# Kernel tuning notes

Hardware: AMD Instinct MI355X
Metric: run time of the kernel (lower is better)

Reference implementation:

```python
import jax, jax.numpy as jnp
import numpy as np

NUM_SINK = 8   # cfg.SINKHORN_ITERS
MASS = 0.9     # marginal value used for a and b


def _graph_conv(x, W_enc, b_enc, W1, b1, W2, b2, k):
    # Node encoder
    h = jax.nn.relu(x @ W_enc + b_enc)                       # [G,M,D]
    # kNN in embedding space (per graph)
    sq = jnp.sum(h * h, axis=-1)                             # [G,M]
    d2 = sq[:, :, None] + sq[:, None, :] - 2.0 * jnp.einsum('gmd,gnd->gmn', h, h)
    d2 = d2 + jnp.eye(h.shape[1], dtype=h.dtype) * 1e9       # exclude self-loop
    _, idx = jax.lax.top_k(-d2, k)                           # [G,M,k]
    neigh = jax.vmap(lambda hg, ig: hg[ig])(h, idx)          # [G,M,k,D]
    hc = jnp.broadcast_to(h[:, :, None, :], neigh.shape)
    e = jnp.concatenate([hc, neigh - hc], axis=-1)           # [G,M,k,2D]
    e = jax.nn.relu(e @ W1 + b1)                             # edge embed
    e = e @ W2 + b2                                          # back to D
    return jnp.max(e, axis=2)                                # max-aggregate over neighbors


def _sinkhorn(cost, lam):
    # log-domain unrolled Sinkhorn, batched over graphs; a=b=0.9 marginals
    log_p = -cost / lam                                      # [G,M,N]
    log_m = jnp.log(jnp.asarray(MASS, cost.dtype))
    for _ in range(NUM_SINK - 1):
        log_p = log_p - (jax.nn.logsumexp(log_p, axis=2, keepdims=True) - log_m)
        log_p = log_p - (jax.nn.logsumexp(log_p, axis=1, keepdims=True) - log_m)
    log_p = log_p - (jax.nn.logsumexp(log_p, axis=2, keepdims=True) - log_m)
    return jnp.exp(log_p)


def setup_inputs() -> dict:
    key = jax.random.key(0)
    ks = jax.random.split(key, 6)
    G, M, D = 64, 256, 256
    E = 256  # edge embed size
    inp = {
        'tra_x': jax.random.normal(ks[0], (G, M, D), jnp.float32),
        'det_x': jax.random.normal(ks[1], (G, M, D), jnp.float32),
        'W_enc': jax.random.normal(ks[2], (D, D), jnp.float32) / np.sqrt(D),
        'b_enc': jnp.zeros((D,), jnp.float32),
        'W1': jax.random.normal(ks[3], (2 * D, E), jnp.float32) / np.sqrt(2 * D),
        'b1': jnp.zeros((E,), jnp.float32),
        'W2': jax.random.normal(ks[4], (E, D), jnp.float32) / np.sqrt(E),
        'b2': jnp.zeros((D,), jnp.float32),
        'eplison': jnp.zeros((1,), jnp.float32),
        'k': 16,
    }
    return inp


def reference(tra_x, det_x, W_enc, b_enc, W1, b1, W2, b2, eplison, k):
    tra = _graph_conv(tra_x, W_enc, b_enc, W1, b1, W2, b2, k)  # [G,M,D]
    det = _graph_conv(det_x, W_enc, b_enc, W1, b1, W2, b2, k)  # [G,N,D]
    corr = jnp.einsum('gmd,gnd->gmn', tra, det)
    n1 = jnp.linalg.norm(tra, axis=-1)                         # [G,M]
    n2 = jnp.linalg.norm(det, axis=-1)                         # [G,N]
    cost = -corr / (n1[:, :, None] * n2[:, None, :])
    lam = jnp.exp(eplison[0]) + 0.03
    return _sinkhorn(cost, lam)                                # [G,M,N]
```

## Files before the change

### kernel.cpp

```cpp
#include <hip/hip_runtime.h>
#include <math.h>

#define NG 64
#define NM 256
#define ND 256
#define NK 16
#define NR (NG * NM)
#define NB 32

#define MASSF 0.9f

typedef _Float16 f16;
typedef __attribute__((ext_vector_type(8))) _Float16 f16x8;
typedef __attribute__((ext_vector_type(4))) _Float16 f16x4;
typedef __attribute__((ext_vector_type(4))) float f32x4;
typedef __attribute__((ext_vector_type(4))) unsigned u32x4;

static __device__ __forceinline__ unsigned pkrelu(unsigned a, unsigned b) {
  unsigned r;
  asm("v_pk_add_f16 %0, %1, %2" : "=v"(r) : "v"(a), "v"(b));
  asm("v_pk_max_f16 %0, %1, %2" : "=v"(r) : "v"(r), "v"(0u));
  return r;
}

__global__ __launch_bounds__(256) void prep_k(const float* __restrict__ W1,
                                              const float* __restrict__ b1,
                                              const float* __restrict__ W2,
                                              f16* __restrict__ w2t, f16* __restrict__ w1cat,
                                              float* __restrict__ biascat) {
  const int b = blockIdx.x, k = threadIdx.x;
  if (b < 256) {
    w2t[b * 256 + k] = (f16)W2[(size_t)k * 256 + b];
  } else {
    const int n = b - 256;
    float v;
    if (n < 256)
      v = W1[(size_t)k * 256 + n] - W1[(size_t)(k + 256) * 256 + n];
    else
      v = W1[(size_t)(k + 256) * 256 + (n - 256)];
    w1cat[(size_t)n * 256 + k] = (f16)v;
    if (k == 0) biascat[n] = (n < 256) ? b1[n] : 0.f;
  }
}

__global__ __launch_bounds__(256) void gemm_nn2_k(const float* __restrict__ A,
                                                  const float* __restrict__ B,
                                                  const float* __restrict__ bias,
                                                  float* __restrict__ C,
                                                  f16* __restrict__ Cf) {
  __shared__ float As[2][16][68];
  __shared__ float Bs[2][16][128];
  const int tid = threadIdx.x;
  const int tx = tid & 15, ty = tid >> 4;
  const int m0 = blockIdx.y * 64, n0 = blockIdx.x * 128;
  const int arow = tid >> 2, akc = (tid & 3) * 4;
  const int bkr = tid >> 4, bcc = (tid & 15) * 4;
  float4 av, bv0, bv1;
  float acc[4][8] = {};
  auto gload = [&](int k0) {
    av = *(const float4*)&A[(size_t)(m0 + arow) * 256 + k0 + akc];
    bv0 = *(const float4*)&B[(size_t)(k0 + bkr) * 256 + n0 + bcc];
    bv1 = *(const float4*)&B[(size_t)(k0 + bkr) * 256 + n0 + 64 + bcc];
  };
  auto swrite = [&](int buf) {
    As[buf][akc + 0][arow] = av.x;
    As[buf][akc + 1][arow] = av.y;
    As[buf][akc + 2][arow] = av.z;
    As[buf][akc + 3][arow] = av.w;
    *(float4*)&Bs[buf][bkr][bcc] = bv0;
    *(float4*)&Bs[buf][bkr][64 + bcc] = bv1;
  };
  gload(0);
  swrite(0);
  __syncthreads();
  for (int s = 0; s < 16; ++s) {
    if (s < 15) gload((s + 1) * 16);
    const int buf = s & 1;
#pragma unroll
    for (int kk = 0; kk < 16; ++kk) {
      const float4 a0 = *(const float4*)&As[buf][kk][ty * 4];
      const float4 b0 = *(const float4*)&Bs[buf][kk][tx * 4];
      const float4 b1 = *(const float4*)&Bs[buf][kk][64 + tx * 4];
      const float aa[4] = {a0.x, a0.y, a0.z, a0.w};
      const float bb[8] = {b0.x, b0.y, b0.z, b0.w, b1.x, b1.y, b1.z, b1.w};
#pragma unroll
      for (int i = 0; i < 4; ++i)
#pragma unroll
        for (int j = 0; j < 8; ++j) acc[i][j] = fmaf(aa[i], bb[j], acc[i][j]);
    }
    if (s < 15) swrite((s + 1) & 1);
    __syncthreads();
  }
  const float4 bia0 = *(const float4*)&bias[n0 + tx * 4];
  const float4 bia1 = *(const float4*)&bias[n0 + 64 + tx * 4];
#pragma unroll
  for (int i = 0; i < 4; ++i) {
    const size_t row = (size_t)(m0 + ty * 4 + i);
    float4 o0 = {fmaxf(acc[i][0] + bia0.x, 0.f), fmaxf(acc[i][1] + bia0.y, 0.f),
                 fmaxf(acc[i][2] + bia0.z, 0.f), fmaxf(acc[i][3] + bia0.w, 0.f)};
    float4 o1 = {fmaxf(acc[i][4] + bia1.x, 0.f), fmaxf(acc[i][5] + bia1.y, 0.f),
                 fmaxf(acc[i][6] + bia1.z, 0.f), fmaxf(acc[i][7] + bia1.w, 0.f)};
    *(float4*)&C[row * 256 + n0 + tx * 4] = o0;
    *(float4*)&C[row * 256 + n0 + 64 + tx * 4] = o1;
    f16x4 h0 = {(f16)o0.x, (f16)o0.y, (f16)o0.z, (f16)o0.w};
    f16x4 h1 = {(f16)o1.x, (f16)o1.y, (f16)o1.z, (f16)o1.w};
    *(f16x4*)&Cf[row * 256 + n0 + tx * 4] = h0;
    *(f16x4*)&Cf[row * 256 + n0 + 64 + tx * 4] = h1;
  }
}

__global__ __launch_bounds__(256) void gemm_nt2_k(const float* __restrict__ h,
                                                  float* __restrict__ C,
                                                  float* __restrict__ sq) {
  const int flat0 = blockIdx.x + 2 * (blockIdx.y + 4 * blockIdx.z);
  const int flat = ((flat0 & 7) << 6) | (flat0 >> 3);
  const int bx = flat & 1, by = (flat >> 1) & 3, g = flat >> 3;
  if (bx == 0 && by >= 2) return;
  __shared__ float As[2][16][68];
  __shared__ float Bs[2][16][128];
  const float* Ag = h + (size_t)g * NM * ND;
  float* Cg = C + (size_t)g * NM * NM;
  const int tid = threadIdx.x;
  const int tx = tid & 15, ty = tid >> 4;
  const int m0 = by * 64, n0 = bx * 128;
  const int arow = tid >> 2, akc = (tid & 3) * 4;
  const int brow = tid >> 1, bkc = (tid & 1) * 8;
  float4 av, bva, bvb;
  float acc[4][8] = {};
  auto gload = [&](int k0) {
    av = *(const float4*)&Ag[(size_t)(m0 + arow) * 256 + k0 + akc];
    bva = *(const float4*)&Ag[(size_t)(n0 + brow) * 256 + k0 + bkc];
    bvb = *(const float4*)&Ag[(size_t)(n0 + brow) * 256 + k0 + bkc + 4];
  };
  auto swrite = [&](int buf) {
    As[buf][akc + 0][arow] = av.x;
    As[buf][akc + 1][arow] = av.y;
    As[buf][akc + 2][arow] = av.z;
    As[buf][akc + 3][arow] = av.w;
    Bs[buf][bkc + 0][brow] = bva.x;
    Bs[buf][bkc + 1][brow] = bva.y;
    Bs[buf][bkc + 2][brow] = bva.z;
    Bs[buf][bkc + 3][brow] = bva.w;
    Bs[buf][bkc + 4][brow] = bvb.x;
    Bs[buf][bkc + 5][brow] = bvb.y;
    Bs[buf][bkc + 6][brow] = bvb.z;
    Bs[buf][bkc + 7][brow] = bvb.w;
  };
  gload(0);
  swrite(0);
  __syncthreads();
  for (int s = 0; s < 16; ++s) {
    if (s < 15) gload((s + 1) * 16);
    const int buf = s & 1;
#pragma unroll
    for (int kk = 0; kk < 16; ++kk) {
      const float4 a0 = *(const float4*)&As[buf][kk][ty * 4];
      const float4 b0 = *(const float4*)&Bs[buf][kk][tx * 4];
      const float4 b1 = *(const float4*)&Bs[buf][kk][64 + tx * 4];
      const float aa[4] = {a0.x, a0.y, a0.z, a0.w};
      const float bb[8] = {b0.x, b0.y, b0.z, b0.w, b1.x, b1.y, b1.z, b1.w};
#pragma unroll
      for (int i = 0; i < 4; ++i)
#pragma unroll
        for (int j = 0; j < 8; ++j) acc[i][j] = fmaf(aa[i], bb[j], acc[i][j]);
    }
    if (s < 15) swrite((s + 1) & 1);
    __syncthreads();
  }
  const int c0 = n0 + tx * 4, c1 = n0 + 64 + tx * 4;
#pragma unroll
  for (int i = 0; i < 4; ++i) {
    const int row = m0 + ty * 4 + i;
    float4 o0 = {acc[i][0], acc[i][1], acc[i][2], acc[i][3]};
    float4 o1 = {acc[i][4], acc[i][5], acc[i][6], acc[i][7]};
    *(float4*)&Cg[(size_t)row * 256 + c0] = o0;
    *(float4*)&Cg[(size_t)row * 256 + c1] = o1;
    if (row >= c0 && row < c0 + 4) sq[g * 256 + row] = acc[i][row - c0];
    if (row >= c1 && row < c1 + 4) sq[g * 256 + row] = acc[i][4 + row - c1];
  }
  if (bx == 1 && by < 2) {
#pragma unroll
    for (int j = 0; j < 4; ++j) {
      const size_t col0 = (size_t)(n0 + tx * 4 + j);
      const size_t col1 = (size_t)(n0 + 64 + tx * 4 + j);
      float4 t0 = {acc[0][j], acc[1][j], acc[2][j], acc[3][j]};
      float4 t1 = {acc[0][4 + j], acc[1][4 + j], acc[2][4 + j], acc[3][4 + j]};
      *(float4*)&Cg[col0 * 256 + m0 + ty * 4] = t0;
      *(float4*)&Cg[col1 * 256 + m0 + ty * 4] = t1;
    }
  }
}

__global__ __launch_bounds__(256, 2) void mlp1_mfma_k(const f16* __restrict__ A,
                                                      const f16* __restrict__ Bt,
                                                      const float* __restrict__ biascat,
                                                      f16* __restrict__ baseb,
                                                      f16* __restrict__ n1b) {
  __shared__ char As[64 * 512];
  const int tid = threadIdx.x;
  const int l = tid & 63, wv = tid >> 6;
  const int r = l & 15, gq = l >> 4;
  const int m0 = blockIdx.y * 64, n0 = blockIdx.x * 128;
  f16x8 bfr[2][8];
  float bv[2];
#pragma unroll
  for (int nt = 0; nt < 2; ++nt) {
    const int col = n0 + wv * 32 + nt * 16 + r;
    const f16* wb = Bt + (size_t)col * 256 + gq * 8;
#pragma unroll
    for (int ks = 0; ks < 8; ++ks) bfr[nt][ks] = *(const f16x8*)(wb + ks * 32);
    bv[nt] = biascat[col];
  }
  const int row = tid >> 2, ch = tid & 3;
  const char* ag = (const char*)(A + (size_t)(m0 + row) * 256) + ch * 128;
  char* lb = As + row * 512;
#pragma unroll
  for (int j = 0; j < 8; ++j)
    *(f16x8*)(lb + (((ch * 128 + j * 16)) ^ ((row & 7) << 4))) = *(const f16x8*)(ag + j * 16);
  __syncthreads();
  f32x4 acc[4][2];
#pragma unroll
  for (int mt = 0; mt < 4; ++mt)
#pragma unroll
    for (int nt = 0; nt < 2; ++nt) acc[mt][nt] = (f32x4){0.f, 0.f, 0.f, 0.f};
#pragma unroll
  for (int ks = 0; ks < 8; ++ks) {
    f16x8 a[4];
#pragma unroll
    for (int mt = 0; mt < 4; ++mt)
      a[mt] = *(const f16x8*)(As + (mt * 16 + r) * 512 + ((gq * 16 + ks * 64) ^ ((r & 7) << 4)));
#pragma unroll
    for (int mt = 0; mt < 4; ++mt)
#pragma unroll
      for (int nt = 0; nt < 2; ++nt)
        acc[mt][nt] = __builtin_amdgcn_mfma_f32_16x16x32_f16(a[mt], bfr[nt][ks], acc[mt][nt], 0, 0, 0);
  }
  f16* dst = (n0 < 256) ? baseb : n1b;
  const int cb = (n0 < 256) ? n0 : n0 - 256;
#pragma unroll
  for (int mt = 0; mt < 4; ++mt)
#pragma unroll
    for (int nt = 0; nt < 2; ++nt) {
      const int col = cb + wv * 32 + nt * 16 + r;
#pragma unroll
      for (int reg = 0; reg < 4; ++reg) {
        const int rw = m0 + mt * 16 + gq * 4 + reg;
        dst[(size_t)rw * 256 + col] = (f16)(acc[mt][nt][reg] + bv[nt]);
      }
    }
}

__global__ __launch_bounds__(256, 2) void cost_mfma_k(const f16* __restrict__ featT,
                                                      const f16* __restrict__ featD,
                                                      const float* __restrict__ nA,
                                                      const float* __restrict__ nB,
                                                      const float* __restrict__ eps,
                                                      float* __restrict__ P) {
  __shared__ char As[64 * 512];
  const int g = blockIdx.z;
  const f16* A = featT + (size_t)g * NM * ND;
  const f16* Bt = featD + (size_t)g * NM * ND;
  const int tid = threadIdx.x;
  const int l = tid & 63, wv = tid >> 6;
  const int r = l & 15, gq = l >> 4;
  const int m0 = blockIdx.y * 64, n0 = blockIdx.x * 128;
  f16x8 bfr[2][8];
  float rnb[2];
#pragma unroll
  for (int nt = 0; nt < 2; ++nt) {
    const int col = n0 + wv * 32 + nt * 16 + r;
    const f16* wb = Bt + (size_t)col * 256 + gq * 8;
#pragma unroll
    for (int ks = 0; ks < 8; ++ks) bfr[nt][ks] = *(const f16x8*)(wb + ks * 32);
    rnb[nt] = 1.0f / nB[g * NM + col];
  }
  const int row = tid >> 2, ch = tid & 3;
  const char* ag = (const char*)(A + (size_t)(m0 + row) * 256) + ch * 128;
  char* lb = As + row * 512;
#pragma unroll
  for (int j = 0; j < 8; ++j)
    *(f16x8*)(lb + (((ch * 128 + j * 16)) ^ ((row & 7) << 4))) = *(const f16x8*)(ag + j * 16);
  __syncthreads();
  f32x4 acc[4][2];
#pragma unroll
  for (int mt = 0; mt < 4; ++mt)
#pragma unroll
    for (int nt = 0; nt < 2; ++nt) acc[mt][nt] = (f32x4){0.f, 0.f, 0.f, 0.f};
#pragma unroll
  for (int ks = 0; ks < 8; ++ks) {
    f16x8 a[4];
#pragma unroll
    for (int mt = 0; mt < 4; ++mt)
      a[mt] = *(const f16x8*)(As + (mt * 16 + r) * 512 + ((gq * 16 + ks * 64) ^ ((r & 7) << 4)));
#pragma unroll
    for (int mt = 0; mt < 4; ++mt)
#pragma unroll
      for (int nt = 0; nt < 2; ++nt)
        acc[mt][nt] = __builtin_amdgcn_mfma_f32_16x16x32_f16(a[mt], bfr[nt][ks], acc[mt][nt], 0, 0, 0);
  }
  const float inv_lam = 1.0f / (expf(eps[0]) + 0.03f);
#pragma unroll
  for (int mt = 0; mt < 4; ++mt) {
    float ria[4];
#pragma unroll
    for (int reg = 0; reg < 4; ++reg)
      ria[reg] = inv_lam / nA[g * NM + m0 + mt * 16 + gq * 4 + reg];
#pragma unroll
    for (int nt = 0; nt < 2; ++nt) {
      const int col = n0 + wv * 32 + nt * 16 + r;
#pragma unroll
      for (int reg = 0; reg < 4; ++reg) {
        const int rw = m0 + mt * 16 + gq * 4 + reg;
        P[(size_t)g * NM * NM + (size_t)rw * 256 + col] =
            expf(acc[mt][nt][reg] * ria[reg] * rnb[nt]);
      }
    }
  }
}

__global__ __launch_bounds__(256) void topk_k(const float* __restrict__ S,
                                              const float* __restrict__ sq,
                                              int* __restrict__ idx) {
  const int w = threadIdx.x >> 6, lane = threadIdx.x & 63;
  const int row = blockIdx.x * 4 + w;
  const int g = row >> 8, m = row & 255;
  const float* Srow = S + (size_t)row * NM;
  const float* sqg = sq + g * NM;
  const float sm = sqg[m];
  const float4 sv = *(const float4*)&Srow[lane * 4];
  const float4 qv = *(const float4*)&sqg[lane * 4];
  float cand[4] = {sm + qv.x - 2.f * sv.x, sm + qv.y - 2.f * sv.y, sm + qv.z - 2.f * sv.z,
                   sm + qv.w - 2.f * sv.w};
#pragma unroll
  for (int t = 0; t < 4; ++t)
    if (lane * 4 + t == m) cand[t] = 1e30f;
  for (int rnd = 0; rnd < NK; ++rnd) {
    float bvv = cand[0];
    int bi = lane * 4;
#pragma unroll
    for (int t = 1; t < 4; ++t)
      if (cand[t] < bvv) {
        bvv = cand[t];
        bi = lane * 4 + t;
      }
#pragma unroll
    for (int off = 1; off < 64; off <<= 1) {
      const float ov = __shfl_xor(bvv, off);
      const int oi = __shfl_xor(bi, off);
      if (ov < bvv || (ov == bvv && oi < bi)) {
        bvv = ov;
        bi = oi;
      }
    }
    if (lane == 0) idx[(size_t)row * NK + rnd] = bi;
    if ((bi >> 2) == lane) cand[bi & 3] = 1e30f;
  }
}

__global__ __launch_bounds__(512, 4) void edgemlp_mfma8_k(
    const f16* __restrict__ baseb, const f16* __restrict__ n1b, const int* __restrict__ idx,
    const f16* __restrict__ w2t, const float* __restrict__ b2, f16* __restrict__ featf,
    float* __restrict__ nrm) {
  __shared__ unsigned E[2][2][512 * 4];
  __shared__ int sidx[NB * NK];
  __shared__ float normp[NB][8];
  const int tid = threadIdx.x;
  const int l = tid & 63, wv = tid >> 6;
  const int blk = ((blockIdx.x & 7) << 6) | (blockIdx.x >> 3);
  const int node0 = blk * NB;
  const int g = node0 >> 8;
  const int r = l & 15, gq = l >> 4;
  sidx[tid] = idx[(size_t)node0 * NK + tid];
  f16x8 bfr[2][8];
  float b2v[2];
#pragma unroll
  for (int t = 0; t < 2; ++t) {
    const int nb = wv * 2 + t;
    const f16* wb = w2t + (size_t)(nb * 16 + r) * 256 + gq * 8;
#pragma unroll
    for (int ks = 0; ks < 8; ++ks) bfr[t][ks] = *(const f16x8*)(wb + ks * 32);
    b2v[t] = b2[nb * 16 + r];
  }
  __syncthreads();
  const int r_s = tid & 15;
  const int col_s = ((tid >> 6) * 32) + (((tid >> 4) & 3) * 8);
  u32x4 bs0, ns0, bs1, ns1;
  auto sload = [&](int s) {
    const int na = s * 2;
    bs0 = *(const u32x4*)(baseb + (((size_t)(node0 + na)) << 8) + col_s);
    ns0 = *(const u32x4*)(n1b + ((((size_t)g << 8) + sidx[na * NK + r_s]) << 8) + col_s);
    bs1 = *(const u32x4*)(baseb + (((size_t)(node0 + na + 1)) << 8) + col_s);
    ns1 = *(const u32x4*)(n1b + ((((size_t)g << 8) + sidx[(na + 1) * NK + r_s]) << 8) + col_s);
  };
  auto swrite = [&](int s) {
    const int buf = s & 1;
    u32x4 w0, w1;
#pragma unroll
    for (int q = 0; q < 4; ++q) {
      w0[q] = pkrelu(bs0[q], ns0[q]);
      w1[q] = pkrelu(bs1[q], ns1[q]);
    }
    *(u32x4*)&E[buf][0][tid * 4] = w0;
    *(u32x4*)&E[buf][1][tid * 4] = w1;
  };
  sload(0);
  swrite(0);
  __syncthreads();
  for (int s = 0; s < NB / 2; ++s) {
    if (s + 1 < NB / 2) sload(s + 1);
    const int buf = s & 1;
#pragma unroll
    for (int q = 0; q < 2; ++q) {
      const char* eb = (const char*)&E[buf][q][0];
      f32x4 acc0 = (f32x4){0.f, 0.f, 0.f, 0.f};
      f32x4 acc1 = (f32x4){0.f, 0.f, 0.f, 0.f};
#pragma unroll
      for (int ks = 0; ks < 8; ++ks) {
        const f16x8 a = *(const f16x8*)(eb + ks * 1024 + l * 16);
        acc0 = __builtin_amdgcn_mfma_f32_16x16x32_f16(a, bfr[0][ks], acc0, 0, 0, 0);
        acc1 = __builtin_amdgcn_mfma_f32_16x16x32_f16(a, bfr[1][ks], acc1, 0, 0, 0);
      }
      const int nd = node0 + s * 2 + q;
      float m0v = fmaxf(fmaxf(acc0[0], acc0[1]), fmaxf(acc0[2], acc0[3]));
      m0v = fmaxf(m0v, __shfl_xor(m0v, 16));
      m0v = fmaxf(m0v, __shfl_xor(m0v, 32));
      float m1v = fmaxf(fmaxf(acc1[0], acc1[1]), fmaxf(acc1[2], acc1[3]));
      m1v = fmaxf(m1v, __shfl_xor(m1v, 16));
      m1v = fmaxf(m1v, __shfl_xor(m1v, 32));
      const f16 h0 = (f16)(m0v + b2v[0]);
      const f16 h1 = (f16)(m1v + b2v[1]);
      if (gq == 0) {
        featf[((size_t)nd << 8) + (wv * 2 + 0) * 16 + r] = h0;
        featf[((size_t)nd << 8) + (wv * 2 + 1) * 16 + r] = h1;
      }
      const float o0 = (float)h0, o1 = (float)h1;
      float ss = o0 * o0 + o1 * o1;
      ss += __shfl_xor(ss, 1);
      ss += __shfl_xor(ss, 2);
      ss += __shfl_xor(ss, 4);
      ss += __shfl_xor(ss, 8);
      if (l == 0) normp[s * 2 + q][wv] = ss;
    }
    if (s + 1 < NB / 2) swrite(s + 1);
    __syncthreads();
  }
  if (tid < NB) {
    float s = 0.f;
#pragma unroll
    for (int w = 0; w < 8; ++w) s += normp[tid][w];
    nrm[node0 + tid] = sqrtf(s);
  }
}

__global__ __launch_bounds__(1024) void sinkhorn_k(float* __restrict__ P) {
  __shared__ float red[16][256];
  __shared__ float scal[256];
  const int t = threadIdx.x;
  const int tc = t & 15;
  const int trw = t >> 4;
  const int wv = t >> 6, l = t & 63;
  float* Pg = P + (size_t)blockIdx.x * NM * NM;
  float p[4][16];
#pragma unroll
  for (int i = 0; i < 4; ++i)
#pragma unroll
    for (int q = 0; q < 4; ++q)
      *(f32x4*)&p[i][q * 4] = *(const f32x4*)&Pg[(size_t)(trw * 4 + i) * NM + tc * 16 + q * 4];

  auto rowpass = [&]() {
#pragma unroll
    for (int i = 0; i < 4; ++i) {
      float s = p[i][0];
#pragma unroll
      for (int j = 1; j < 16; ++j) s += p[i][j];
      s += __shfl_xor(s, 1);
      s += __shfl_xor(s, 2);
      s += __shfl_xor(s, 4);
      s += __shfl_xor(s, 8);
      const float sc = MASSF / s;
#pragma unroll
      for (int j = 0; j < 16; ++j) p[i][j] *= sc;
    }
  };
  auto colpass = [&]() {
    float tmp[16];
#pragma unroll
    for (int j = 0; j < 16; ++j) tmp[j] = ((p[0][j] + p[1][j]) + (p[2][j] + p[3][j]));
#pragma unroll
    for (int j = 0; j < 16; ++j) {
      tmp[j] += __shfl_xor(tmp[j], 16);
      tmp[j] += __shfl_xor(tmp[j], 32);
    }
    if (l < 16) {
#pragma unroll
      for (int q = 0; q < 4; ++q)
        *(f32x4*)&red[wv][l * 16 + q * 4] = *(const f32x4*)&tmp[q * 4];
    }
    __syncthreads();
    if (t < 256) {
      float s = red[0][t];
#pragma unroll
      for (int w = 1; w < 16; ++w) s += red[w][t];
      scal[t] = MASSF / s;
    }
    __syncthreads();
#pragma unroll
    for (int j = 0; j < 16; ++j) {
      const float sc = scal[tc * 16 + j];
#pragma unroll
      for (int i = 0; i < 4; ++i) p[i][j] *= sc;
    }
    __syncthreads();
  };
  for (int it = 0; it < 7; ++it) {
    rowpass();
    colpass();
  }
  rowpass();
#pragma unroll
  for (int i = 0; i < 4; ++i)
#pragma unroll
    for (int q = 0; q < 4; ++q)
      *(f32x4*)&Pg[(size_t)(trw * 4 + i) * NM + tc * 16 + q * 4] = *(const f32x4*)&p[i][q * 4];
}

extern "C" void kernel_launch(void* const* d_in, const int* in_sizes, int n_in, void* d_out,
                              int out_size, void* d_ws, size_t ws_size, hipStream_t stream) {
  const float* tra_x = (const float*)d_in[0];
  const float* det_x = (const float*)d_in[1];
  const float* W_enc = (const float*)d_in[2];
  const float* b_enc = (const float*)d_in[3];
  const float* W1 = (const float*)d_in[4];
  const float* b1 = (const float*)d_in[5];
  const float* W2 = (const float*)d_in[6];
  const float* b2 = (const float*)d_in[7];
  const float* eps = (const float*)d_in[8];
  float* out = (float*)d_out;

  const size_t SZ = (size_t)NR * ND;
  float* h = (float*)d_ws;
  f16* hf = (f16*)(h + SZ);
  f16* baseb = hf + SZ;
  f16* n1b = baseb + SZ;
  f16* featT = n1b + SZ;
  f16* featD = featT + SZ;
  float* sq = (float*)(featD + SZ);
  float* nT = sq + NR;
  float* nD = nT + NR;
  int* idx = (int*)(nD + NR);
  f16* w2t = (f16*)(idx + (size_t)NR * NK);
  f16* w1cat = w2t + 256 * 256;
  float* biascat = (float*)(w1cat + 512 * 256);
  float* S = out;

  const float* xs[2] = {tra_x, det_x};
  f16* feats[2] = {featT, featD};
  float* nrms[2] = {nT, nD};

  prep_k<<<768, 256, 0, stream>>>(W1, b1, W2, w2t, w1cat, biascat);
  for (int s2 = 0; s2 < 2; ++s2) {
    gemm_nn2_k<<<dim3(2, 256), 256, 0, stream>>>(xs[s2], W_enc, b_enc, h, hf);
    mlp1_mfma_k<<<dim3(4, 256), 256, 0, stream>>>(hf, w1cat, biascat, baseb, n1b);
    gemm_nt2_k<<<dim3(2, 4, NG), 256, 0, stream>>>(h, S, sq);
    topk_k<<<4096, 256, 0, stream>>>(S, sq, idx);
    edgemlp_mfma8_k<<<NR / NB, 512, 0, stream>>>(baseb, n1b, idx, w2t, b2, feats[s2], nrms[s2]);
  }
  cost_mfma_k<<<dim3(2, 4, NG), 256, 0, stream>>>(featT, featD, nT, nD, eps, out);
  sinkhorn_k<<<NG, 1024, 0, stream>>>(out);
}
```

Baseline: 377.7 us.

## Widen FP32 GEMM tiles, batch edge MLP over both graphs, swizzle cost grid

The encoder GEMM and pairwise-distance GEMM now use full 256-column tiles with 8x8 per-thread accumulators, which cuts grid size and A-tile reloads. The distance GEMM drops its symmetric half-tile trick and computes the full square. Workspace buffers for the edge MLP inputs and the kNN indices are doubled so a single edge-MLP launch covers both graphs. The cost kernel gets an XCD-style block swizzle. The larger register tiles and strided scalar stores may hurt occupancy and store coalescing, and the redundant symmetric compute adds work.

```diff
diff --git a/kernel.cpp b/kernel.cpp
--- a/kernel.cpp
+++ b/kernel.cpp
@@ -43,32 +43,33 @@
   }
 }
 
-__global__ __launch_bounds__(256) void gemm_nn2_k(const float* __restrict__ A,
+__global__ __launch_bounds__(256) void gemm_nn3_k(const float* __restrict__ A,
                                                   const float* __restrict__ B,
                                                   const float* __restrict__ bias,
                                                   float* __restrict__ C,
                                                   f16* __restrict__ Cf) {
   __shared__ float As[2][16][68];
-  __shared__ float Bs[2][16][128];
+  __shared__ float Bs[2][16][264];
   const int tid = threadIdx.x;
-  const int tx = tid & 15, ty = tid >> 4;
-  const int m0 = blockIdx.y * 64, n0 = blockIdx.x * 128;
+  const int tx = tid & 31, ty = tid >> 5;
+  const int m0 = blockIdx.x * 64;
   const int arow = tid >> 2, akc = (tid & 3) * 4;
-  const int bkr = tid >> 4, bcc = (tid & 15) * 4;
-  float4 av, bv0, bv1;
-  float acc[4][8] = {};
+  const int bkr = tid >> 4, bcc = (tid & 15) * 16;
+  float4 av, bv[4];
+  float acc[8][8] = {};
   auto gload = [&](int k0) {
     av = *(const float4*)&A[(size_t)(m0 + arow) * 256 + k0 + akc];
-    bv0 = *(const float4*)&B[(size_t)(k0 + bkr) * 256 + n0 + bcc];
-    bv1 = *(const float4*)&B[(size_t)(k0 + bkr) * 256 + n0 + 64 + bcc];
+#pragma unroll
+    for (int q = 0; q < 4; ++q)
+      bv[q] = *(const float4*)&B[(size_t)(k0 + bkr) * 256 + bcc + q * 4];
   };
   auto swrite = [&](int buf) {
     As[buf][akc + 0][arow] = av.x;
     As[buf][akc + 1][arow] = av.y;
     As[buf][akc + 2][arow] = av.z;
     As[buf][akc + 3][arow] = av.w;
-    *(float4*)&Bs[buf][bkr][bcc] = bv0;
-    *(float4*)&Bs[buf][bkr][64 + bcc] = bv1;
+#pragma unroll
+    for (int q = 0; q < 4; ++q) *(float4*)&Bs[buf][bkr][bcc + q * 4] = bv[q];
   };
   gload(0);
   swrite(0);
@@ -78,73 +79,68 @@
     const int buf = s & 1;
 #pragma unroll
     for (int kk = 0; kk < 16; ++kk) {
-      const float4 a0 = *(const float4*)&As[buf][kk][ty * 4];
-      const float4 b0 = *(const float4*)&Bs[buf][kk][tx * 4];
-      const float4 b1 = *(const float4*)&Bs[buf][kk][64 + tx * 4];
-      const float aa[4] = {a0.x, a0.y, a0.z, a0.w};
-      const float bb[8] = {b0.x, b0.y, b0.z, b0.w, b1.x, b1.y, b1.z, b1.w};
-#pragma unroll
-      for (int i = 0; i < 4; ++i)
+      float aa[8], bb[8];
+      *(float4*)&aa[0] = *(const float4*)&As[buf][kk][ty * 8];
+      *(float4*)&aa[4] = *(const float4*)&As[buf][kk][ty * 8 + 4];
+#pragma unroll
+      for (int j = 0; j < 8; ++j) bb[j] = Bs[buf][kk][tx + 32 * j];
+#pragma unroll
+      for (int i = 0; i < 8; ++i)
 #pragma unroll
         for (int j = 0; j < 8; ++j) acc[i][j] = fmaf(aa[i], bb[j], acc[i][j]);
     }
     if (s < 15) swrite((s + 1) & 1);
     __syncthreads();
   }
-  const float4 bia0 = *(const float4*)&bias[n0 + tx * 4];
-  const float4 bia1 = *(const float4*)&bias[n0 + 64 + tx * 4];
-#pragma unroll
-  for (int i = 0; i < 4; ++i) {
-    const size_t row = (size_t)(m0 + ty * 4 + i);
-    float4 o0 = {fmaxf(acc[i][0] + bia0.x, 0.f), fmaxf(acc[i][1] + bia0.y, 0.f),
-                 fmaxf(acc[i][2] + bia0.z, 0.f), fmaxf(acc[i][3] + bia0.w, 0.f)};
-    float4 o1 = {fmaxf(acc[i][4] + bia1.x, 0.f), fmaxf(acc[i][5] + bia1.y, 0.f),
-                 fmaxf(acc[i][6] + bia1.z, 0.f), fmaxf(acc[i][7] + bia1.w, 0.f)};
-    *(float4*)&C[row * 256 + n0 + tx * 4] = o0;
-    *(float4*)&C[row * 256 + n0 + 64 + tx * 4] = o1;
-    f16x4 h0 = {(f16)o0.x, (f16)o0.y, (f16)o0.z, (f16)o0.w};
-    f16x4 h1 = {(f16)o1.x, (f16)o1.y, (f16)o1.z, (f16)o1.w};
-    *(f16x4*)&Cf[row * 256 + n0 + tx * 4] = h0;
-    *(f16x4*)&Cf[row * 256 + n0 + 64 + tx * 4] = h1;
-  }
-}
-
-__global__ __launch_bounds__(256) void gemm_nt2_k(const float* __restrict__ h,
+  float bi[8];
+#pragma unroll
+  for (int j = 0; j < 8; ++j) bi[j] = bias[tx + 32 * j];
+#pragma unroll
+  for (int i = 0; i < 8; ++i) {
+    const size_t row = (size_t)(m0 + ty * 8 + i);
+#pragma unroll
+    for (int j = 0; j < 8; ++j) {
+      const float o = fmaxf(acc[i][j] + bi[j], 0.f);
+      C[row * 256 + tx + 32 * j] = o;
+      Cf[row * 256 + tx + 32 * j] = (f16)o;
+    }
+  }
+}
+
+__global__ __launch_bounds__(256) void gemm_nt3_k(const float* __restrict__ h,
                                                   float* __restrict__ C,
                                                   float* __restrict__ sq) {
-  const int flat0 = blockIdx.x + 2 * (blockIdx.y + 4 * blockIdx.z);
-  const int flat = ((flat0 & 7) << 6) | (flat0 >> 3);
-  const int bx = flat & 1, by = (flat >> 1) & 3, g = flat >> 3;
-  if (bx == 0 && by >= 2) return;
+  const int flat0 = blockIdx.x + 4 * blockIdx.y;
+  const int flat = ((flat0 & 7) << 5) | (flat0 >> 3);
+  const int by = flat & 3, g = flat >> 2;
   __shared__ float As[2][16][68];
-  __shared__ float Bs[2][16][128];
+  __shared__ float Bs[2][16][264];
   const float* Ag = h + (size_t)g * NM * ND;
   float* Cg = C + (size_t)g * NM * NM;
   const int tid = threadIdx.x;
-  const int tx = tid & 15, ty = tid >> 4;
-  const int m0 = by * 64, n0 = bx * 128;
+  const int tx = tid & 31, ty = tid >> 5;
+  const int m0 = by * 64;
   const int arow = tid >> 2, akc = (tid & 3) * 4;
-  const int brow = tid >> 1, bkc = (tid & 1) * 8;
-  float4 av, bva, bvb;
-  float acc[4][8] = {};
+  float4 av, bv[4];
+  float acc[8][8] = {};
   auto gload = [&](int k0) {
     av = *(const float4*)&Ag[(size_t)(m0 + arow) * 256 + k0 + akc];
-    bva = *(const float4*)&Ag[(size_t)(n0 + brow) * 256 + k0 + bkc];
-    bvb = *(const float4*)&Ag[(size_t)(n0 + brow) * 256 + k0 + bkc + 4];
+#pragma unroll
+    for (int q = 0; q < 4; ++q)
+      bv[q] = *(const float4*)&Ag[(size_t)tid * 256 + k0 + q * 4];
   };
   auto swrite = [&](int buf) {
     As[buf][akc + 0][arow] = av.x;
     As[buf][akc + 1][arow] = av.y;
     As[buf][akc + 2][arow] = av.z;
     As[buf][akc + 3][arow] = av.w;
-    Bs[buf][bkc + 0][brow] = bva.x;
-    Bs[buf][bkc + 1][brow] = bva.y;
-    Bs[buf][bkc + 2][brow] = bva.z;
-    Bs[buf][bkc + 3][brow] = bva.w;
-    Bs[buf][bkc + 4][brow] = bvb.x;
-    Bs[buf][bkc + 5][brow] = bvb.y;
-    Bs[buf][bkc + 6][brow] = bvb.z;
-    Bs[buf][bkc + 7][brow] = bvb.w;
+#pragma unroll
+    for (int q = 0; q < 4; ++q) {
+      Bs[buf][q * 4 + 0][tid] = bv[q].x;
+      Bs[buf][q * 4 + 1][tid] = bv[q].y;
+      Bs[buf][q * 4 + 2][tid] = bv[q].z;
+      Bs[buf][q * 4 + 3][tid] = bv[q].w;
+    }
   };
   gload(0);
   swrite(0);
@@ -154,39 +150,27 @@
     const int buf = s & 1;
 #pragma unroll
     for (int kk = 0; kk < 16; ++kk) {
-      const float4 a0 = *(const float4*)&As[buf][kk][ty * 4];
-      const float4 b0 = *(const float4*)&Bs[buf][kk][tx * 4];
-      const float4 b1 = *(const float4*)&Bs[buf][kk][64 + tx * 4];
-      const float aa[4] = {a0.x, a0.y, a0.z, a0.w};
-      const float bb[8] = {b0.x, b0.y, b0.z, b0.w, b1.x, b1.y, b1.z, b1.w};
-#pragma unroll
-      for (int i = 0; i < 4; ++i)
+      float aa[8], bb[8];
+      *(float4*)&aa[0] = *(const float4*)&As[buf][kk][ty * 8];
+      *(float4*)&aa[4] = *(const float4*)&As[buf][kk][ty * 8 + 4];
+#pragma unroll
+      for (int j = 0; j < 8; ++j) bb[j] = Bs[buf][kk][tx + 32 * j];
+#pragma unroll
+      for (int i = 0; i < 8; ++i)
 #pragma unroll
         for (int j = 0; j < 8; ++j) acc[i][j] = fmaf(aa[i], bb[j], acc[i][j]);
     }
     if (s < 15) swrite((s + 1) & 1);
     __syncthreads();
   }
-  const int c0 = n0 + tx * 4, c1 = n0 + 64 + tx * 4;
-#pragma unroll
-  for (int i = 0; i < 4; ++i) {
-    const int row = m0 + ty * 4 + i;
-    float4 o0 = {acc[i][0], acc[i][1], acc[i][2], acc[i][3]};
-    float4 o1 = {acc[i][4], acc[i][5], acc[i][6], acc[i][7]};
-    *(float4*)&Cg[(size_t)row * 256 + c0] = o0;
-    *(float4*)&Cg[(size_t)row * 256 + c1] = o1;
-    if (row >= c0 && row < c0 + 4) sq[g * 256 + row] = acc[i][row - c0];
-    if (row >= c1 && row < c1 + 4) sq[g * 256 + row] = acc[i][4 + row - c1];
-  }
-  if (bx == 1 && by < 2) {
-#pragma unroll
-    for (int j = 0; j < 4; ++j) {
-      const size_t col0 = (size_t)(n0 + tx * 4 + j);
-      const size_t col1 = (size_t)(n0 + 64 + tx * 4 + j);
-      float4 t0 = {acc[0][j], acc[1][j], acc[2][j], acc[3][j]};
-      float4 t1 = {acc[0][4 + j], acc[1][4 + j], acc[2][4 + j], acc[3][4 + j]};
-      *(float4*)&Cg[col0 * 256 + m0 + ty * 4] = t0;
-      *(float4*)&Cg[col1 * 256 + m0 + ty * 4] = t1;
+#pragma unroll
+  for (int i = 0; i < 8; ++i) {
+    const int row = m0 + ty * 8 + i;
+#pragma unroll
+    for (int j = 0; j < 8; ++j) {
+      const int col = tx + 32 * j;
+      Cg[(size_t)row * 256 + col] = acc[i][j];
+      if (row == col) sq[g * 256 + row] = acc[i][j];
     }
   }
 }
@@ -257,13 +241,14 @@
                                                       const float* __restrict__ eps,
                                                       float* __restrict__ P) {
   __shared__ char As[64 * 512];
-  const int g = blockIdx.z;
+  const int flat = ((blockIdx.x & 7) << 6) | (blockIdx.x >> 3);
+  const int bx = flat & 1, by = (flat >> 1) & 3, g = flat >> 3;
   const f16* A = featT + (size_t)g * NM * ND;
   const f16* Bt = featD + (size_t)g * NM * ND;
   const int tid = threadIdx.x;
   const int l = tid & 63, wv = tid >> 6;
   const int r = l & 15, gq = l >> 4;
-  const int m0 = blockIdx.y * 64, n0 = blockIdx.x * 128;
+  const int m0 = by * 64, n0 = bx * 128;
   f16x8 bfr[2][8];
   float rnb[2];
 #pragma unroll
@@ -357,18 +342,27 @@
   }
 }
 
-__global__ __launch_bounds__(512, 4) void edgemlp_mfma8_k(
-    const f16* __restrict__ baseb, const f16* __restrict__ n1b, const int* __restrict__ idx,
-    const f16* __restrict__ w2t, const float* __restrict__ b2, f16* __restrict__ featf,
-    float* __restrict__ nrm) {
+__global__ __launch_bounds__(512, 4) void edgemlp_mfma10_k(
+    const f16* __restrict__ baseb2, const f16* __restrict__ n1b2, const int* __restrict__ idx2,
+    const f16* __restrict__ w2t, const float* __restrict__ b2, f16* __restrict__ featf2,
+    float* __restrict__ nrm2) {
   __shared__ unsigned E[2][2][512 * 4];
   __shared__ int sidx[NB * NK];
   __shared__ float normp[NB][8];
   const int tid = threadIdx.x;
   const int l = tid & 63, wv = tid >> 6;
-  const int blk = ((blockIdx.x & 7) << 6) | (blockIdx.x >> 3);
+  const size_t SZH = (size_t)NR * ND;
+  const int bid = blockIdx.x;
+  const int half = bid >> 9;
+  const int b9 = bid & 511;
+  const int blk = ((b9 & 7) << 6) | (b9 >> 3);
   const int node0 = blk * NB;
   const int g = node0 >> 8;
+  const f16* baseb = baseb2 + (size_t)half * SZH;
+  const f16* n1b = n1b2 + (size_t)half * SZH;
+  const int* idx = idx2 + (size_t)half * NR * NK;
+  f16* featf = featf2 + (size_t)half * SZH;
+  float* nrm = nrm2 + (size_t)half * NR;
   const int r = l & 15, gq = l >> 4;
   sidx[tid] = idx[(size_t)node0 * NK + tid];
   f16x8 bfr[2][8];
@@ -541,30 +535,29 @@
   float* h = (float*)d_ws;
   f16* hf = (f16*)(h + SZ);
   f16* baseb = hf + SZ;
-  f16* n1b = baseb + SZ;
-  f16* featT = n1b + SZ;
+  f16* n1b = baseb + 2 * SZ;
+  f16* featT = n1b + 2 * SZ;
   f16* featD = featT + SZ;
   float* sq = (float*)(featD + SZ);
   float* nT = sq + NR;
   float* nD = nT + NR;
   int* idx = (int*)(nD + NR);
-  f16* w2t = (f16*)(idx + (size_t)NR * NK);
+  f16* w2t = (f16*)(idx + 2 * (size_t)NR * NK);
   f16* w1cat = w2t + 256 * 256;
   float* biascat = (float*)(w1cat + 512 * 256);
   float* S = out;
 
   const float* xs[2] = {tra_x, det_x};
-  f16* feats[2] = {featT, featD};
-  float* nrms[2] = {nT, nD};
 
   prep_k<<<768, 256, 0, stream>>>(W1, b1, W2, w2t, w1cat, biascat);
   for (int s2 = 0; s2 < 2; ++s2) {
-    gemm_nn2_k<<<dim3(2, 256), 256, 0, stream>>>(xs[s2], W_enc, b_enc, h, hf);
-    mlp1_mfma_k<<<dim3(4, 256), 256, 0, stream>>>(hf, w1cat, biascat, baseb, n1b);
-    gemm_nt2_k<<<dim3(2, 4, NG), 256, 0, stream>>>(h, S, sq);
-    topk_k<<<4096, 256, 0, stream>>>(S, sq, idx);
-    edgemlp_mfma8_k<<<NR / NB, 512, 0, stream>>>(baseb, n1b, idx, w2t, b2, feats[s2], nrms[s2]);
-  }
-  cost_mfma_k<<<dim3(2, 4, NG), 256, 0, stream>>>(featT, featD, nT, nD, eps, out);
+    gemm_nn3_k<<<256, 256, 0, stream>>>(xs[s2], W_enc, b_enc, h, hf);
+    mlp1_mfma_k<<<dim3(4, 256), 256, 0, stream>>>(hf, w1cat, biascat, baseb + s2 * SZ,
+                                                  n1b + s2 * SZ);
+    gemm_nt3_k<<<dim3(4, 64), 256, 0, stream>>>(h, S, sq);
+    topk_k<<<4096, 256, 0, stream>>>(S, sq, idx + (size_t)s2 * NR * NK);
+  }
+  edgemlp_mfma10_k<<<1024, 512, 0, stream>>>(baseb, n1b, idx, w2t, b2, featT, nT);
+  cost_mfma_k<<<512, 256, 0, stream>>>(featT, featD, nT, nD, eps, out);
   sinkhorn_k<<<NG, 1024, 0, stream>>>(out);
 }
```

After: 439.5 us. 16.4% more time.
